# Kernel tuning notes

Measured on AMD Instinct MI355X. Metric: run time of the kernel, lower is better.

The kernel has to match this reference:

```python
import jax, jax.numpy as jnp
import numpy as np

N_NODES = 20000
N_EDGES = 640000
HIDDEN = 128


def setup_inputs() -> dict:
    key = jax.random.key(0)
    k1, k2, k3, k4 = jax.random.split(key, 4)
    scale = 1.0 / np.sqrt(HIDDEN)
    features = jax.random.normal(k1, (N_NODES, HIDDEN), dtype=jnp.float32)
    edge_index = jax.random.randint(k2, (2, N_EDGES), 0, N_NODES, dtype=jnp.int64)
    W_l = jax.random.normal(k3, (HIDDEN, HIDDEN), dtype=jnp.float32) * scale
    b_l = jnp.zeros((HIDDEN,), dtype=jnp.float32)
    W_r = jax.random.normal(k4, (HIDDEN, HIDDEN), dtype=jnp.float32) * scale
    return {"features": features, "edge_index": edge_index, "W_l": W_l, "b_l": b_l, "W_r": W_r}


def reference(features, edge_index, W_l, b_l, W_r):
    # PyG SAGEConv with mean aggregation:
    #   out_i = lin_l(mean_{j : (j->i) in E} x_j) + lin_r(x_i)
    # edge_index[0] = source nodes, edge_index[1] = target nodes.
    n = features.shape[0]
    src = edge_index[0]
    dst = edge_index[1]
    msg = features[src]  # [E, d] gather
    summed = jax.ops.segment_sum(msg, dst, num_segments=n)  # [N, d] scatter-add
    cnt = jax.ops.segment_sum(jnp.ones(src.shape[0], dtype=features.dtype), dst, num_segments=n)
    agg = summed / jnp.maximum(cnt, 1.0)[:, None]  # mean; isolated nodes -> 0
    return agg @ W_l.T + b_l + features @ W_r.T
```

## Files before the change

kernel.cpp:

```cpp
#include <hip/hip_runtime.h>

#define N_NODES 20000
#define N_EDGES 640000
#define HIDDEN  128
#define CAP     96
#define DEG_PAD 16

typedef unsigned short bf16_t;

__device__ __forceinline__ bf16_t f2bf(float f) {
    union { float f; unsigned int i; } v; v.f = f;
    unsigned int x = v.i + 0x7FFFu + ((v.i >> 16) & 1u);
    return (bf16_t)(x >> 16);
}
__device__ __forceinline__ float bf2f(bf16_t u) {
    union { unsigned int i; float f; } v; v.i = ((unsigned int)u) << 16; return v.f;
}
__device__ __forceinline__ float bflo(unsigned u) {
    union { unsigned i; float f; } v; v.i = u << 16; return v.f;
}
__device__ __forceinline__ float bfhi(unsigned u) {
    union { unsigned i; float f; } v; v.i = u & 0xFFFF0000u; return v.f;
}
__device__ __forceinline__ unsigned pack2(float x, float y) {
    return (unsigned)f2bf(x) | ((unsigned)f2bf(y) << 16);
}

__global__ void prep_kernel(const float* __restrict__ feat,
                            const float* __restrict__ Wl,
                            const float* __restrict__ Wr,
                            bf16_t* __restrict__ feat_bf,
                            float* __restrict__ Wt) {
    int t = blockIdx.x * 256 + threadIdx.x;
    if (t < (N_NODES * HIDDEN) / 4) {
        float4 v = ((const float4*)feat)[t];
        ushort4 o = { f2bf(v.x), f2bf(v.y), f2bf(v.z), f2bf(v.w) };
        ((ushort4*)feat_bf)[t] = o;
    }
    if (t < 2 * HIDDEN * HIDDEN) {
        int k = t >> 7, j = t & 127;
        Wt[t] = (k < HIDDEN) ? Wl[j * HIDDEN + k] : Wr[j * HIDDEN + (k - HIDDEN)];
    }
}

__global__ void bucket_fill_kernel(const int* __restrict__ eidx,
                                   int* __restrict__ deg,
                                   int* __restrict__ bucket) {
    int e = blockIdx.x * 256 + threadIdx.x;
    if (e >= N_EDGES) return;
    int src = eidx[e];
    int dst = eidx[N_EDGES + e];
    int pos = atomicAdd(&deg[dst * DEG_PAD], 1);
    if (pos < CAP) bucket[dst * CAP + pos] = src;
}

__global__ __launch_bounds__(256) void gather_kernel(
        const bf16_t* __restrict__ feat_bf,
        const int* __restrict__ deg,
        const int* __restrict__ bucket,
        bf16_t* __restrict__ agg_bf) {
    int wid  = (blockIdx.x * 256 + threadIdx.x) >> 6;
    int lane = threadIdx.x & 63;
    if (wid >= N_NODES) return;
    int d_true = deg[wid * DEG_PAD];
    int d = min(d_true, CAP);
    const int* row = bucket + wid * CAP;
    const unsigned* f = (const unsigned*)feat_bf;
    float ax0=0,ay0=0, ax1=0,ay1=0, ax2=0,ay2=0, ax3=0,ay3=0;
    int i = 0;
    for (; i + 4 <= d; i += 4) {
        int4 s = *(const int4*)(row + i);
        unsigned u0 = f[s.x * 64 + lane];
        unsigned u1 = f[s.y * 64 + lane];
        unsigned u2 = f[s.z * 64 + lane];
        unsigned u3 = f[s.w * 64 + lane];
        ax0 += bflo(u0); ay0 += bfhi(u0);
        ax1 += bflo(u1); ay1 += bfhi(u1);
        ax2 += bflo(u2); ay2 += bfhi(u2);
        ax3 += bflo(u3); ay3 += bfhi(u3);
    }
    for (; i < d; ++i) {
        unsigned u = f[row[i] * 64 + lane];
        ax0 += bflo(u); ay0 += bfhi(u);
    }
    float inv = 1.0f / fmaxf((float)d_true, 1.0f);
    float x = (ax0 + ax1 + ax2 + ax3) * inv;
    float y = (ay0 + ay1 + ay2 + ay3) * inv;
    ((unsigned*)agg_bf)[wid * 64 + lane] = pack2(x, y);
}

__global__ __launch_bounds__(256) void gemm_kernel(
        const bf16_t* __restrict__ agg_bf,
        const bf16_t* __restrict__ feat_bf,
        const float* __restrict__ Wt,
        const float* __restrict__ bl,
        float* __restrict__ out) {
    __shared__ float As[32][72];
    __shared__ float Bs[32][128];

    const int t = threadIdx.x;
    const int row0 = blockIdx.x * 64;
    const int col0 = (t & 31) * 4;
    const int rgrp = (t >> 5) * 8;

    float acc[8][4];
#pragma unroll
    for (int r = 0; r < 8; ++r)
#pragma unroll
        for (int c = 0; c < 4; ++c) acc[r][c] = 0.0f;

    for (int kt = 0; kt < 8; ++kt) {
        const int ksrc = kt * 32;
        {
            const float4* s4 = (const float4*)(Wt + ksrc * 128);
            float4* d4 = (float4*)(&Bs[0][0]);
#pragma unroll
            for (int i = 0; i < 4; ++i) d4[t + 256 * i] = s4[t + 256 * i];
        }
#pragma unroll
        for (int i = 0; i < 2; ++i) {
            int fid = t * 2 + i;
            int rl  = fid >> 3;
            int kb  = fid & 7;
            int row = row0 + rl;
            float4 v = {0.f, 0.f, 0.f, 0.f};
            if (row < N_NODES) {
                const bf16_t* srcp = (ksrc < 128) ? agg_bf : feat_bf;
                ushort4 u = ((const ushort4*)srcp)[row * 32 + ((ksrc & 127) >> 2) + kb];
                v.x = bf2f(u.x); v.y = bf2f(u.y); v.z = bf2f(u.z); v.w = bf2f(u.w);
            }
            int kk = kb * 4;
            As[kk + 0][rl] = v.x;
            As[kk + 1][rl] = v.y;
            As[kk + 2][rl] = v.z;
            As[kk + 3][rl] = v.w;
        }
        __syncthreads();

#pragma unroll
        for (int kk = 0; kk < 32; ++kk) {
            float4 b  = *(const float4*)&Bs[kk][col0];
            float4 a0 = *(const float4*)&As[kk][rgrp];
            float4 a1 = *(const float4*)&As[kk][rgrp + 4];
            float a[8] = {a0.x, a0.y, a0.z, a0.w, a1.x, a1.y, a1.z, a1.w};
#pragma unroll
            for (int r = 0; r < 8; ++r) {
                acc[r][0] = fmaf(a[r], b.x, acc[r][0]);
                acc[r][1] = fmaf(a[r], b.y, acc[r][1]);
                acc[r][2] = fmaf(a[r], b.z, acc[r][2]);
                acc[r][3] = fmaf(a[r], b.w, acc[r][3]);
            }
        }
        __syncthreads();
    }

    float4 bias = ((const float4*)bl)[t & 31];
#pragma unroll
    for (int r = 0; r < 8; ++r) {
        int row = row0 + rgrp + r;
        if (row < N_NODES) {
            float4 o;
            o.x = acc[r][0] + bias.x;
            o.y = acc[r][1] + bias.y;
            o.z = acc[r][2] + bias.z;
            o.w = acc[r][3] + bias.w;
            ((float4*)out)[row * 32 + (t & 31)] = o;
        }
    }
}

extern "C" void kernel_launch(void* const* d_in, const int* in_sizes, int n_in,
                              void* d_out, int out_size, void* d_ws, size_t ws_size,
                              hipStream_t stream) {
    const float* feat = (const float*)d_in[0];
    const int*   eidx = (const int*)d_in[1];
    const float* Wl   = (const float*)d_in[2];
    const float* bl   = (const float*)d_in[3];
    const float* Wr   = (const float*)d_in[4];
    float* out = (float*)d_out;

    int*    deg     = (int*)d_ws;
    int*    bucket  = deg + N_NODES * DEG_PAD;
    float*  Wt      = (float*)(bucket + N_NODES * CAP);
    bf16_t* feat_bf = (bf16_t*)(Wt + 2 * HIDDEN * HIDDEN);
    bf16_t* agg_bf  = feat_bf + (size_t)N_NODES * HIDDEN;

    hipMemsetAsync(deg, 0, (size_t)N_NODES * DEG_PAD * sizeof(int), stream);

    prep_kernel<<<2500, 256, 0, stream>>>(feat, Wl, Wr, feat_bf, Wt);
    bucket_fill_kernel<<<(N_EDGES + 255) / 256, 256, 0, stream>>>(eidx, deg, bucket);
    gather_kernel<<<(N_NODES * 64 + 255) / 256, 256, 0, stream>>>(feat_bf, deg, bucket, agg_bf);
    gemm_kernel<<<(N_NODES + 63) / 64, 256, 0, stream>>>(agg_bf, feat_bf, Wt, bl, out);
}
```

Measured before the change: 160.6 us.

## Replace FP32 tiled GEMM with bf16 MFMA kernel and prepacked weight fragments

```diff
diff --git a/kernel.cpp b/kernel.cpp
--- a/kernel.cpp
+++ b/kernel.cpp
@@ -7,14 +7,13 @@
 #define DEG_PAD 16
 
 typedef unsigned short bf16_t;
+typedef __attribute__((ext_vector_type(8))) short short8;
+typedef __attribute__((ext_vector_type(4))) float floatx4;
 
 __device__ __forceinline__ bf16_t f2bf(float f) {
     union { float f; unsigned int i; } v; v.f = f;
     unsigned int x = v.i + 0x7FFFu + ((v.i >> 16) & 1u);
     return (bf16_t)(x >> 16);
-}
-__device__ __forceinline__ float bf2f(bf16_t u) {
-    union { unsigned int i; float f; } v; v.i = ((unsigned int)u) << 16; return v.f;
 }
 __device__ __forceinline__ float bflo(unsigned u) {
     union { unsigned i; float f; } v; v.i = u << 16; return v.f;
@@ -30,7 +29,7 @@
                             const float* __restrict__ Wl,
                             const float* __restrict__ Wr,
                             bf16_t* __restrict__ feat_bf,
-                            float* __restrict__ Wt) {
+                            bf16_t* __restrict__ Bp) {
     int t = blockIdx.x * 256 + threadIdx.x;
     if (t < (N_NODES * HIDDEN) / 4) {
         float4 v = ((const float4*)feat)[t];
@@ -38,8 +37,14 @@
         ((ushort4*)feat_bf)[t] = o;
     }
     if (t < 2 * HIDDEN * HIDDEN) {
-        int k = t >> 7, j = t & 127;
-        Wt[t] = (k < HIDDEN) ? Wl[j * HIDDEN + k] : Wr[j * HIDDEN + (k - HIDDEN)];
+        int j    = t & 7;
+        int lane = (t >> 3) & 63;
+        int nt   = (t >> 9) & 7;
+        int kt   = t >> 12;
+        int n = nt * 16 + (lane & 15);
+        int k = kt * 32 + (lane >> 4) * 8 + j;
+        float v = (k < HIDDEN) ? Wl[n * HIDDEN + k] : Wr[n * HIDDEN + (k - HIDDEN)];
+        Bp[t] = f2bf(v);
     }
 }
 
@@ -89,82 +94,45 @@
     ((unsigned*)agg_bf)[wid * 64 + lane] = pack2(x, y);
 }
 
-__global__ __launch_bounds__(256) void gemm_kernel(
+__global__ __launch_bounds__(256) void gemm_mfma_kernel(
         const bf16_t* __restrict__ agg_bf,
         const bf16_t* __restrict__ feat_bf,
-        const float* __restrict__ Wt,
+        const bf16_t* __restrict__ Bp,
         const float* __restrict__ bl,
         float* __restrict__ out) {
-    __shared__ float As[32][72];
-    __shared__ float Bs[32][128];
+    int wid = blockIdx.x * 4 + (threadIdx.x >> 6);
+    if (wid >= N_NODES / 16) return;
+    int lane = threadIdx.x & 63;
+    int m    = lane & 15;
+    int quad = lane >> 4;
+    int row0 = wid * 16;
 
-    const int t = threadIdx.x;
-    const int row0 = blockIdx.x * 64;
-    const int col0 = (t & 31) * 4;
-    const int rgrp = (t >> 5) * 8;
+    floatx4 acc[8];
+    floatx4 z = {0.f, 0.f, 0.f, 0.f};
+#pragma unroll
+    for (int nt = 0; nt < 8; ++nt) acc[nt] = z;
 
-    float acc[8][4];
+    const short8* bp = (const short8*)Bp;
 #pragma unroll
-    for (int r = 0; r < 8; ++r)
+    for (int kt = 0; kt < 8; ++kt) {
+        const bf16_t* asrc = (kt < 4) ? agg_bf : feat_bf;
+        int koff = (kt & 3) * 32 + quad * 8;
+        short8 afrag = *(const short8*)(asrc + (size_t)(row0 + m) * HIDDEN + koff);
 #pragma unroll
-        for (int c = 0; c < 4; ++c) acc[r][c] = 0.0f;
-
-    for (int kt = 0; kt < 8; ++kt) {
-        const int ksrc = kt * 32;
-        {
-            const float4* s4 = (const float4*)(Wt + ksrc * 128);
-            float4* d4 = (float4*)(&Bs[0][0]);
-#pragma unroll
-            for (int i = 0; i < 4; ++i) d4[t + 256 * i] = s4[t + 256 * i];
+        for (int nt = 0; nt < 8; ++nt) {
+            short8 bfrag = bp[(kt * 8 + nt) * 64 + lane];
+            acc[nt] = __builtin_amdgcn_mfma_f32_16x16x32_bf16(afrag, bfrag, acc[nt], 0, 0, 0);
         }
-#pragma unroll
-        for (int i = 0; i < 2; ++i) {
-            int fid = t * 2 + i;
-            int rl  = fid >> 3;
-            int kb  = fid & 7;
-            int row = row0 + rl;
-            float4 v = {0.f, 0.f, 0.f, 0.f};
-            if (row < N_NODES) {
-                const bf16_t* srcp = (ksrc < 128) ? agg_bf : feat_bf;
-                ushort4 u = ((const ushort4*)srcp)[row * 32 + ((ksrc & 127) >> 2) + kb];
-                v.x = bf2f(u.x); v.y = bf2f(u.y); v.z = bf2f(u.z); v.w = bf2f(u.w);
-            }
-            int kk = kb * 4;
-            As[kk + 0][rl] = v.x;
-            As[kk + 1][rl] = v.y;
-            As[kk + 2][rl] = v.z;
-            As[kk + 3][rl] = v.w;
-        }
-        __syncthreads();
-
-#pragma unroll
-        for (int kk = 0; kk < 32; ++kk) {
-            float4 b  = *(const float4*)&Bs[kk][col0];
-            float4 a0 = *(const float4*)&As[kk][rgrp];
-            float4 a1 = *(const float4*)&As[kk][rgrp + 4];
-            float a[8] = {a0.x, a0.y, a0.z, a0.w, a1.x, a1.y, a1.z, a1.w};
-#pragma unroll
-            for (int r = 0; r < 8; ++r) {
-                acc[r][0] = fmaf(a[r], b.x, acc[r][0]);
-                acc[r][1] = fmaf(a[r], b.y, acc[r][1]);
-                acc[r][2] = fmaf(a[r], b.z, acc[r][2]);
-                acc[r][3] = fmaf(a[r], b.w, acc[r][3]);
-            }
-        }
-        __syncthreads();
     }
 
-    float4 bias = ((const float4*)bl)[t & 31];
+    int col = lane & 15;
 #pragma unroll
-    for (int r = 0; r < 8; ++r) {
-        int row = row0 + rgrp + r;
-        if (row < N_NODES) {
-            float4 o;
-            o.x = acc[r][0] + bias.x;
-            o.y = acc[r][1] + bias.y;
-            o.z = acc[r][2] + bias.z;
-            o.w = acc[r][3] + bias.w;
-            ((float4*)out)[row * 32 + (t & 31)] = o;
+    for (int nt = 0; nt < 8; ++nt) {
+        float b = bl[nt * 16 + col];
+#pragma unroll
+        for (int r = 0; r < 4; ++r) {
+            int row = row0 + quad * 4 + r;
+            out[(size_t)row * HIDDEN + nt * 16 + col] = acc[nt][r] + b;
         }
     }
 }
@@ -181,14 +149,14 @@
 
     int*    deg     = (int*)d_ws;
     int*    bucket  = deg + N_NODES * DEG_PAD;
-    float*  Wt      = (float*)(bucket + N_NODES * CAP);
-    bf16_t* feat_bf = (bf16_t*)(Wt + 2 * HIDDEN * HIDDEN);
+    bf16_t* Bp      = (bf16_t*)(bucket + N_NODES * CAP);
+    bf16_t* feat_bf = Bp + 2 * HIDDEN * HIDDEN;
     bf16_t* agg_bf  = feat_bf + (size_t)N_NODES * HIDDEN;
 
     hipMemsetAsync(deg, 0, (size_t)N_NODES * DEG_PAD * sizeof(int), stream);
 
-    prep_kernel<<<2500, 256, 0, stream>>>(feat, Wl, Wr, feat_bf, Wt);
+    prep_kernel<<<2500, 256, 0, stream>>>(feat, Wl, Wr, feat_bf, Bp);
     bucket_fill_kernel<<<(N_EDGES + 255) / 256, 256, 0, stream>>>(eidx, deg, bucket);
     gather_kernel<<<(N_NODES * 64 + 255) / 256, 256, 0, stream>>>(feat_bf, deg, bucket, agg_bf);
-    gemm_kernel<<<(N_NODES + 63) / 64, 256, 0, stream>>>(agg_bf, feat_bf, Wt, bl, out);
+    gemm_mfma_kernel<<<(N_NODES / 16 + 3) / 4, 256, 0, stream>>>(agg_bf, feat_bf, Bp, bl, out);
 }
```

New measurement: 140.1 us. -12.8%, faster.
